# Kernel tuning notes

Hardware: AMD Instinct MI355X
Metric: run time of the kernel (lower is better)

Reference implementation:

```python
import jax, jax.numpy as jnp
import numpy as np

E = 128   # embedding_dim
H = 8     # num_attention_heads
D = 16    # head_size = E // H


def setup_inputs() -> dict:
    key = jax.random.key(0)
    ks = jax.random.split(key, 7)
    B, N = 2, 512
    x = jax.random.normal(ks[0], (B, N, E), jnp.float32)
    e = jax.random.uniform(ks[1], (B, N, N), jnp.float32)  # dense pairwise edge weights
    s_qkv = 1.0 / np.sqrt(D)
    w_qkv = jax.random.uniform(ks[2], (3 * H * D, E), jnp.float32, -s_qkv, s_qkv)
    w_ekv = jax.random.normal(ks[3], (2 * H * D, 1), jnp.float32) * 1.0
    b_ekv = jax.random.normal(ks[4], (2 * H * D,), jnp.float32) * 0.01
    s_prj = 1.0 / np.sqrt(E)
    w_prj = jax.random.uniform(ks[5], (E, H * D), jnp.float32, -s_prj, s_prj)
    b_prj = jnp.zeros((E,), jnp.float32)
    return {"x": x, "e": e, "w_qkv": w_qkv, "w_ekv": w_ekv,
            "b_ekv": b_ekv, "w_prj": w_prj, "b_prj": b_prj}


def reference(x, e, w_qkv, w_ekv, b_ekv, w_prj, b_prj):
    B, N, _ = x.shape
    # qkv projection: [B,N,3*H*D] split per einops '(S H D)'
    qkv = (x @ w_qkv.T).reshape(B, N, 3, H, D)
    q = jnp.transpose(qkv[:, :, 0], (0, 2, 1, 3))  # [B,H,N,D]
    k = jnp.transpose(qkv[:, :, 1], (0, 2, 1, 3))  # [B,H,N,D]
    v = jnp.transpose(qkv[:, :, 2], (0, 2, 1, 3))  # [B,H,N,D]
    # edge-conditioned K/V biases: Linear(1 -> 2HD) + LeakyReLU(0.01)
    ekv = jax.nn.leaky_relu(e[..., None] * w_ekv[:, 0] + b_ekv)  # [B,N,M,2HD]
    ekv = ekv.reshape(B, N, N, 2, H, D)
    ekm = jnp.transpose(ekv[..., 0, :, :], (0, 3, 1, 2, 4))  # [B,H,N,M,D]
    evm = jnp.transpose(ekv[..., 1, :, :], (0, 3, 1, 2, 4))  # [B,H,N,M,D]
    # dots[b,h,n,m] = q[b,h,n] . (k[b,h,n] + ekm[b,h,n,m])
    # NOTE: original uses the key of the *query* node n (broadcast over m).
    dots = jnp.sum(q * k, axis=-1)[..., None] \
        + jnp.einsum('bhnd,bhnmd->bhnm', q, ekm)
    attn = jax.nn.softmax(dots / np.sqrt(D), axis=-1)  # [B,H,N,M]
    # hat[b,h,n] = sum_m attn * (v[b,h,n] + evm[b,h,n,m])
    hat = v * jnp.sum(attn, axis=-1)[..., None] \
        + jnp.einsum('bhnm,bhnmd->bhnd', attn, evm)  # [B,H,N,D]
    out = jnp.transpose(hat, (0, 2, 1, 3)).reshape(B, N, H * D) @ w_prj.T + b_prj
    return out
```

## Files before the change

kernel.cpp:

```cpp
#include <hip/hip_runtime.h>
#include <math.h>

#define BATCH 2
#define NSEQ  512
#define EDIM  128
#define HNUM  8
#define DDIM  16
#define MROWS (BATCH*NSEQ)

__global__ __launch_bounds__(256)
void qkv_gemm(const float* __restrict__ x, const float* __restrict__ w,
              float* __restrict__ qkv) {
    __shared__ float4 As[32 * 32];
    __shared__ float4 Bs[64 * 32];

    const int tid  = threadIdx.x;
    const int row0 = blockIdx.y * 32;
    const int col0 = blockIdx.x * 64;

    #pragma unroll
    for (int it = 0; it < 4; ++it) {
        int idx = tid + it * 256;
        int r = idx >> 5, k4 = idx & 31;
        As[r * 32 + (k4 ^ ((r >> 2) & 7))] =
            ((const float4*)(x + (size_t)(row0 + r) * 128))[k4];
    }
    #pragma unroll
    for (int it = 0; it < 8; ++it) {
        int idx = tid + it * 256;
        int r = idx >> 5, k4 = idx & 31;
        Bs[r * 32 + (k4 ^ ((r >> 2) & 7))] =
            ((const float4*)(w + (size_t)(col0 + r) * 128))[k4];
    }
    __syncthreads();

    const int ty = tid >> 4;
    const int tx = tid & 15;
    const int ra  = ty * 2;
    const int swa = (ra >> 2) & 7;
    const int rb  = tx * 4;
    const int swb = tx & 7;

    float acc[2][4] = {};
    #pragma unroll
    for (int k4 = 0; k4 < 32; ++k4) {
        float4 a0 = As[ ra      * 32 + (k4 ^ swa)];
        float4 a1 = As[(ra + 1) * 32 + (k4 ^ swa)];
        float4 bv[4];
        #pragma unroll
        for (int j = 0; j < 4; ++j)
            bv[j] = Bs[(rb + j) * 32 + (k4 ^ swb)];
        #pragma unroll
        for (int j = 0; j < 4; ++j) {
            acc[0][j] = fmaf(a0.x, bv[j].x, acc[0][j]);
            acc[0][j] = fmaf(a0.y, bv[j].y, acc[0][j]);
            acc[0][j] = fmaf(a0.z, bv[j].z, acc[0][j]);
            acc[0][j] = fmaf(a0.w, bv[j].w, acc[0][j]);
            acc[1][j] = fmaf(a1.x, bv[j].x, acc[1][j]);
            acc[1][j] = fmaf(a1.y, bv[j].y, acc[1][j]);
            acc[1][j] = fmaf(a1.z, bv[j].z, acc[1][j]);
            acc[1][j] = fmaf(a1.w, bv[j].w, acc[1][j]);
        }
    }

    #pragma unroll
    for (int i = 0; i < 2; ++i) {
        float* crow = qkv + (size_t)(row0 + ra + i) * 384 + col0 + rb;
        *(float4*)crow = make_float4(acc[i][0], acc[i][1], acc[i][2], acc[i][3]);
    }
}

__global__ __launch_bounds__(512)
void attn_proj(const float* __restrict__ qkv, const float* __restrict__ e,
               const float* __restrict__ wekv, const float* __restrict__ bekv,
               const float* __restrict__ wprj, const float* __restrict__ bprj,
               float* __restrict__ out) {
    __shared__ float hat_s[EDIM];

    const int tid  = threadIdx.x;
    const int lane = tid & 63;
    const int h    = tid >> 6;
    const int bn   = blockIdx.x;

    const float* qrow = qkv + (size_t)bn * 384 + h * DDIM;
    const float* krow = qrow + EDIM;
    const float* vrow = qrow + 2 * EDIM;
    const float* erow = e + (size_t)bn * NSEQ;

    const float SC = 0.25f * 1.44269504088896340736f;

    float wk[DDIM], bk[DDIM], cd[DDIM];
    float qk = 0.f, qwk = 0.f, qbk = 0.f;
    #pragma unroll
    for (int d = 0; d < DDIM; ++d) {
        float q = qrow[d];
        qk  = fmaf(q, krow[d], qk);
        wk[d] = wekv[h * DDIM + d];
        bk[d] = bekv[h * DDIM + d];
        qwk = fmaf(q, wk[d], qwk);
        qbk = fmaf(q, bk[d], qbk);
        cd[d] = 0.495f * SC * q;
    }
    const float Alin = SC * 0.505f * qwk;
    const float base = SC * (qk + 0.505f * qbk);

    float dots[NSEQ / 64], ev[NSEQ / 64];
    float lmax = -1e30f;
    #pragma unroll
    for (int c = 0; c < NSEQ / 64; ++c) {
        float s = erow[c * 64 + lane];
        ev[c] = s;
        float dot = fmaf(s, Alin, base);
        #pragma unroll
        for (int d = 0; d < DDIM; ++d) {
            float t = fmaf(s, wk[d], bk[d]);
            dot = fmaf(cd[d], fabsf(t), dot);
        }
        dots[c] = dot;
        lmax = fmaxf(lmax, dot);
    }
    #pragma unroll
    for (int off = 32; off >= 1; off >>= 1)
        lmax = fmaxf(lmax, __shfl_xor(lmax, off, 64));

    float wvv[DDIM], bv[DDIM], racc[DDIM];
    #pragma unroll
    for (int d = 0; d < DDIM; ++d) {
        wvv[d]  = wekv[EDIM + h * DDIM + d];
        bv[d]   = bekv[EDIM + h * DDIM + d];
        racc[d] = 0.f;
    }
    float sp = 0.f, spe = 0.f;
    #pragma unroll
    for (int c = 0; c < NSEQ / 64; ++c) {
        float p = __builtin_amdgcn_exp2f(dots[c] - lmax);
        float s = ev[c];
        sp  += p;
        spe  = fmaf(p, s, spe);
        float pm = 0.495f * p;
        #pragma unroll
        for (int d = 0; d < DDIM; ++d) {
            float t = fmaf(s, wvv[d], bv[d]);
            racc[d] = fmaf(pm, fabsf(t), racc[d]);
        }
    }

    #pragma unroll
    for (int off = 1; off < 64; off <<= 1) {
        sp  += __shfl_xor(sp,  off, 64);
        spe += __shfl_xor(spe, off, 64);
        #pragma unroll
        for (int d = 0; d < DDIM; ++d)
            racc[d] += __shfl_xor(racc[d], off, 64);
    }

    float rsel = racc[0];
    #pragma unroll
    for (int d = 1; d < DDIM; ++d) rsel = (lane == d) ? racc[d] : rsel;
    if (lane < DDIM) {
        float wvs = wekv[EDIM + h * DDIM + lane];
        float bvs = bekv[EDIM + h * DDIM + lane];
        float acc = rsel + 0.505f * (fmaf(wvs, spe, bvs * sp));
        hat_s[h * DDIM + lane] = vrow[lane] + acc / sp;
    }
    __syncthreads();

    const int c    = tid >> 2;
    const int quad = tid & 3;
    const float4* wp = (const float4*)(wprj + (size_t)c * EDIM + quad * 32);
    const float4* hp = (const float4*)(hat_s + quad * 32);
    float s = 0.f;
    #pragma unroll
    for (int j = 0; j < 8; ++j) {
        float4 wv4 = wp[j], hv4 = hp[j];
        s = fmaf(wv4.x, hv4.x, s);
        s = fmaf(wv4.y, hv4.y, s);
        s = fmaf(wv4.z, hv4.z, s);
        s = fmaf(wv4.w, hv4.w, s);
    }
    s += __shfl_xor(s, 1, 64);
    s += __shfl_xor(s, 2, 64);
    if (quad == 0)
        out[(size_t)bn * EDIM + c] = s + bprj[c];
}

extern "C" void kernel_launch(void* const* d_in, const int* in_sizes, int n_in,
                              void* d_out, int out_size, void* d_ws, size_t ws_size,
                              hipStream_t stream) {
    const float* x     = (const float*)d_in[0];
    const float* e     = (const float*)d_in[1];
    const float* w_qkv = (const float*)d_in[2];
    const float* w_ekv = (const float*)d_in[3];
    const float* b_ekv = (const float*)d_in[4];
    const float* w_prj = (const float*)d_in[5];
    const float* b_prj = (const float*)d_in[6];
    float* out = (float*)d_out;

    float* qkv = (float*)d_ws;

    qkv_gemm<<<dim3(384 / 64, MROWS / 32), 256, 0, stream>>>(x, w_qkv, qkv);

    attn_proj<<<MROWS, 512, 0, stream>>>(qkv, e, w_ekv, b_ekv, w_prj, b_prj, out);
}
```

Before: 94.11 us.

## Fuse QKV projection into attention kernel, computing per-row GEMV in shared memory

```diff
diff --git a/kernel.cpp b/kernel.cpp
--- a/kernel.cpp
+++ b/kernel.cpp
@@ -8,73 +8,13 @@
 #define DDIM  16
 #define MROWS (BATCH*NSEQ)
 
-__global__ __launch_bounds__(256)
-void qkv_gemm(const float* __restrict__ x, const float* __restrict__ w,
-              float* __restrict__ qkv) {
-    __shared__ float4 As[32 * 32];
-    __shared__ float4 Bs[64 * 32];
-
-    const int tid  = threadIdx.x;
-    const int row0 = blockIdx.y * 32;
-    const int col0 = blockIdx.x * 64;
-
-    #pragma unroll
-    for (int it = 0; it < 4; ++it) {
-        int idx = tid + it * 256;
-        int r = idx >> 5, k4 = idx & 31;
-        As[r * 32 + (k4 ^ ((r >> 2) & 7))] =
-            ((const float4*)(x + (size_t)(row0 + r) * 128))[k4];
-    }
-    #pragma unroll
-    for (int it = 0; it < 8; ++it) {
-        int idx = tid + it * 256;
-        int r = idx >> 5, k4 = idx & 31;
-        Bs[r * 32 + (k4 ^ ((r >> 2) & 7))] =
-            ((const float4*)(w + (size_t)(col0 + r) * 128))[k4];
-    }
-    __syncthreads();
-
-    const int ty = tid >> 4;
-    const int tx = tid & 15;
-    const int ra  = ty * 2;
-    const int swa = (ra >> 2) & 7;
-    const int rb  = tx * 4;
-    const int swb = tx & 7;
-
-    float acc[2][4] = {};
-    #pragma unroll
-    for (int k4 = 0; k4 < 32; ++k4) {
-        float4 a0 = As[ ra      * 32 + (k4 ^ swa)];
-        float4 a1 = As[(ra + 1) * 32 + (k4 ^ swa)];
-        float4 bv[4];
-        #pragma unroll
-        for (int j = 0; j < 4; ++j)
-            bv[j] = Bs[(rb + j) * 32 + (k4 ^ swb)];
-        #pragma unroll
-        for (int j = 0; j < 4; ++j) {
-            acc[0][j] = fmaf(a0.x, bv[j].x, acc[0][j]);
-            acc[0][j] = fmaf(a0.y, bv[j].y, acc[0][j]);
-            acc[0][j] = fmaf(a0.z, bv[j].z, acc[0][j]);
-            acc[0][j] = fmaf(a0.w, bv[j].w, acc[0][j]);
-            acc[1][j] = fmaf(a1.x, bv[j].x, acc[1][j]);
-            acc[1][j] = fmaf(a1.y, bv[j].y, acc[1][j]);
-            acc[1][j] = fmaf(a1.z, bv[j].z, acc[1][j]);
-            acc[1][j] = fmaf(a1.w, bv[j].w, acc[1][j]);
-        }
-    }
-
-    #pragma unroll
-    for (int i = 0; i < 2; ++i) {
-        float* crow = qkv + (size_t)(row0 + ra + i) * 384 + col0 + rb;
-        *(float4*)crow = make_float4(acc[i][0], acc[i][1], acc[i][2], acc[i][3]);
-    }
-}
-
-__global__ __launch_bounds__(512)
-void attn_proj(const float* __restrict__ qkv, const float* __restrict__ e,
-               const float* __restrict__ wekv, const float* __restrict__ bekv,
-               const float* __restrict__ wprj, const float* __restrict__ bprj,
-               float* __restrict__ out) {
+__global__ __launch_bounds__(512, 4)
+void fused_attn(const float* __restrict__ x,    const float* __restrict__ e,
+                const float* __restrict__ wqkv, const float* __restrict__ wekv,
+                const float* __restrict__ bekv, const float* __restrict__ wprj,
+                const float* __restrict__ bprj, float* __restrict__ out) {
+    __shared__ float xs[EDIM];
+    __shared__ float qkvs[3 * EDIM];
     __shared__ float hat_s[EDIM];
 
     const int tid  = threadIdx.x;
@@ -82,10 +22,43 @@
     const int h    = tid >> 6;
     const int bn   = blockIdx.x;
 
-    const float* qrow = qkv + (size_t)bn * 384 + h * DDIM;
+    const float* erow = e + (size_t)bn * NSEQ;
+    float ev[NSEQ / 64];
+    #pragma unroll
+    for (int c = 0; c < NSEQ / 64; ++c)
+        ev[c] = erow[c * 64 + lane];
+
+    if (tid < 32)
+        ((float4*)xs)[tid] = ((const float4*)(x + (size_t)bn * EDIM))[tid];
+    __syncthreads();
+
+    {
+        const int o   = tid >> 2;
+        const int seg = tid & 3;
+        #pragma unroll
+        for (int rep = 0; rep < 3; ++rep) {
+            const int oo = o + rep * 128;
+            const float4* wp = (const float4*)(wqkv + (size_t)oo * EDIM + seg * 32);
+            const float4* xp = (const float4*)(xs + seg * 32);
+            float s = 0.f;
+            #pragma unroll
+            for (int j = 0; j < 8; ++j) {
+                float4 w4 = wp[j], x4 = xp[j];
+                s = fmaf(w4.x, x4.x, s);
+                s = fmaf(w4.y, x4.y, s);
+                s = fmaf(w4.z, x4.z, s);
+                s = fmaf(w4.w, x4.w, s);
+            }
+            s += __shfl_xor(s, 1, 64);
+            s += __shfl_xor(s, 2, 64);
+            if (seg == 0) qkvs[oo] = s;
+        }
+    }
+    __syncthreads();
+
+    const float* qrow = qkvs + h * DDIM;
     const float* krow = qrow + EDIM;
     const float* vrow = qrow + 2 * EDIM;
-    const float* erow = e + (size_t)bn * NSEQ;
 
     const float SC = 0.25f * 1.44269504088896340736f;
 
@@ -104,12 +77,11 @@
     const float Alin = SC * 0.505f * qwk;
     const float base = SC * (qk + 0.505f * qbk);
 
-    float dots[NSEQ / 64], ev[NSEQ / 64];
+    float dots[NSEQ / 64];
     float lmax = -1e30f;
     #pragma unroll
     for (int c = 0; c < NSEQ / 64; ++c) {
-        float s = erow[c * 64 + lane];
-        ev[c] = s;
+        float s = ev[c];
         float dot = fmaf(s, Alin, base);
         #pragma unroll
         for (int d = 0; d < DDIM; ++d) {
@@ -160,7 +132,7 @@
     if (lane < DDIM) {
         float wvs = wekv[EDIM + h * DDIM + lane];
         float bvs = bekv[EDIM + h * DDIM + lane];
-        float acc = rsel + 0.505f * (fmaf(wvs, spe, bvs * sp));
+        float acc = rsel + 0.505f * fmaf(wvs, spe, bvs * sp);
         hat_s[h * DDIM + lane] = vrow[lane] + acc / sp;
     }
     __syncthreads();
@@ -172,11 +144,11 @@
     float s = 0.f;
     #pragma unroll
     for (int j = 0; j < 8; ++j) {
-        float4 wv4 = wp[j], hv4 = hp[j];
-        s = fmaf(wv4.x, hv4.x, s);
-        s = fmaf(wv4.y, hv4.y, s);
-        s = fmaf(wv4.z, hv4.z, s);
-        s = fmaf(wv4.w, hv4.w, s);
+        float4 w4 = wp[j], h4 = hp[j];
+        s = fmaf(w4.x, h4.x, s);
+        s = fmaf(w4.y, h4.y, s);
+        s = fmaf(w4.z, h4.z, s);
+        s = fmaf(w4.w, h4.w, s);
     }
     s += __shfl_xor(s, 1, 64);
     s += __shfl_xor(s, 2, 64);
@@ -196,9 +168,6 @@
     const float* b_prj = (const float*)d_in[6];
     float* out = (float*)d_out;
 
-    float* qkv = (float*)d_ws;
-
-    qkv_gemm<<<dim3(384 / 64, MROWS / 32), 256, 0, stream>>>(x, w_qkv, qkv);
-
-    attn_proj<<<MROWS, 512, 0, stream>>>(qkv, e, w_ekv, b_ekv, w_prj, b_prj, out);
+    fused_attn<<<MROWS, 512, 0, stream>>>(x, e, w_qkv, w_ekv, b_ekv,
+                                          w_prj, b_prj, out);
 }
```

Measured after the change: 102.9 us. 9.4% more time.

## Drop K projection and softmax max pass; reduce racc via LDS transpose

Applied to the files above, without the earlier changes.

```diff
diff --git a/kernel.cpp b/kernel.cpp
--- a/kernel.cpp
+++ b/kernel.cpp
@@ -9,14 +9,16 @@
 #define MROWS (BATCH*NSEQ)
 
 __global__ __launch_bounds__(256)
-void qkv_gemm(const float* __restrict__ x, const float* __restrict__ w,
-              float* __restrict__ qkv) {
+void qv_gemm(const float* __restrict__ x, const float* __restrict__ w,
+             float* __restrict__ qv) {
     __shared__ float4 As[32 * 32];
     __shared__ float4 Bs[64 * 32];
 
     const int tid  = threadIdx.x;
     const int row0 = blockIdx.y * 32;
-    const int col0 = blockIdx.x * 64;
+    const int bx   = blockIdx.x;
+    const int wr0  = (bx >> 1) * 256 + (bx & 1) * 64;
+    const int cc0  = (bx >> 1) * 128 + (bx & 1) * 64;
 
     #pragma unroll
     for (int it = 0; it < 4; ++it) {
@@ -30,12 +32,12 @@
         int idx = tid + it * 256;
         int r = idx >> 5, k4 = idx & 31;
         Bs[r * 32 + (k4 ^ ((r >> 2) & 7))] =
-            ((const float4*)(w + (size_t)(col0 + r) * 128))[k4];
+            ((const float4*)(w + (size_t)(wr0 + r) * 128))[k4];
     }
     __syncthreads();
 
-    const int ty = tid >> 4;
-    const int tx = tid & 15;
+    const int ty  = tid >> 4;
+    const int tx  = tid & 15;
     const int ra  = ty * 2;
     const int swa = (ra >> 2) & 7;
     const int rb  = tx * 4;
@@ -46,102 +48,87 @@
     for (int k4 = 0; k4 < 32; ++k4) {
         float4 a0 = As[ ra      * 32 + (k4 ^ swa)];
         float4 a1 = As[(ra + 1) * 32 + (k4 ^ swa)];
-        float4 bv[4];
+        float4 bv4[4];
         #pragma unroll
         for (int j = 0; j < 4; ++j)
-            bv[j] = Bs[(rb + j) * 32 + (k4 ^ swb)];
+            bv4[j] = Bs[(rb + j) * 32 + (k4 ^ swb)];
         #pragma unroll
         for (int j = 0; j < 4; ++j) {
-            acc[0][j] = fmaf(a0.x, bv[j].x, acc[0][j]);
-            acc[0][j] = fmaf(a0.y, bv[j].y, acc[0][j]);
-            acc[0][j] = fmaf(a0.z, bv[j].z, acc[0][j]);
-            acc[0][j] = fmaf(a0.w, bv[j].w, acc[0][j]);
-            acc[1][j] = fmaf(a1.x, bv[j].x, acc[1][j]);
-            acc[1][j] = fmaf(a1.y, bv[j].y, acc[1][j]);
-            acc[1][j] = fmaf(a1.z, bv[j].z, acc[1][j]);
-            acc[1][j] = fmaf(a1.w, bv[j].w, acc[1][j]);
+            acc[0][j] = fmaf(a0.x, bv4[j].x, acc[0][j]);
+            acc[0][j] = fmaf(a0.y, bv4[j].y, acc[0][j]);
+            acc[0][j] = fmaf(a0.z, bv4[j].z, acc[0][j]);
+            acc[0][j] = fmaf(a0.w, bv4[j].w, acc[0][j]);
+            acc[1][j] = fmaf(a1.x, bv4[j].x, acc[1][j]);
+            acc[1][j] = fmaf(a1.y, bv4[j].y, acc[1][j]);
+            acc[1][j] = fmaf(a1.z, bv4[j].z, acc[1][j]);
+            acc[1][j] = fmaf(a1.w, bv4[j].w, acc[1][j]);
         }
     }
 
     #pragma unroll
     for (int i = 0; i < 2; ++i) {
-        float* crow = qkv + (size_t)(row0 + ra + i) * 384 + col0 + rb;
+        float* crow = qv + (size_t)(row0 + ra + i) * 256 + cc0 + rb;
         *(float4*)crow = make_float4(acc[i][0], acc[i][1], acc[i][2], acc[i][3]);
     }
 }
 
 __global__ __launch_bounds__(512)
-void attn_proj(const float* __restrict__ qkv, const float* __restrict__ e,
+void attn_proj(const float* __restrict__ qv,   const float* __restrict__ e,
                const float* __restrict__ wekv, const float* __restrict__ bekv,
                const float* __restrict__ wprj, const float* __restrict__ bprj,
                float* __restrict__ out) {
     __shared__ float hat_s[EDIM];
+    __shared__ float red[HNUM][DDIM][65];
 
     const int tid  = threadIdx.x;
     const int lane = tid & 63;
-    const int h    = tid >> 6;
+    const int h    = __builtin_amdgcn_readfirstlane(tid >> 6);
     const int bn   = blockIdx.x;
 
-    const float* qrow = qkv + (size_t)bn * 384 + h * DDIM;
-    const float* krow = qrow + EDIM;
-    const float* vrow = qrow + 2 * EDIM;
+    const float* qrow = qv + (size_t)bn * 256 + h * DDIM;
+    const float* vrow = qrow + 128;
     const float* erow = e + (size_t)bn * NSEQ;
 
     const float SC = 0.25f * 1.44269504088896340736f;
 
-    float wk[DDIM], bk[DDIM], cd[DDIM];
-    float qk = 0.f, qwk = 0.f, qbk = 0.f;
+    float wk[DDIM], bk[DDIM], cd[DDIM], wvv[DDIM], bv[DDIM];
+    float qwk = 0.f;
     #pragma unroll
     for (int d = 0; d < DDIM; ++d) {
         float q = qrow[d];
-        qk  = fmaf(q, krow[d], qk);
-        wk[d] = wekv[h * DDIM + d];
-        bk[d] = bekv[h * DDIM + d];
-        qwk = fmaf(q, wk[d], qwk);
-        qbk = fmaf(q, bk[d], qbk);
-        cd[d] = 0.495f * SC * q;
+        wk[d]  = wekv[h * DDIM + d];
+        bk[d]  = bekv[h * DDIM + d];
+        wvv[d] = wekv[EDIM + h * DDIM + d];
+        bv[d]  = bekv[EDIM + h * DDIM + d];
+        qwk    = fmaf(q, wk[d], qwk);
+        cd[d]  = 0.495f * SC * q;
     }
     const float Alin = SC * 0.505f * qwk;
-    const float base = SC * (qk + 0.505f * qbk);
 
-    float dots[NSEQ / 64], ev[NSEQ / 64];
-    float lmax = -1e30f;
+    float4 e0 = ((const float4*)erow)[lane];
+    float4 e1 = ((const float4*)erow)[lane + 64];
+    float evs[8] = {e0.x, e0.y, e0.z, e0.w, e1.x, e1.y, e1.z, e1.w};
+
+    float racc[DDIM];
     #pragma unroll
-    for (int c = 0; c < NSEQ / 64; ++c) {
-        float s = erow[c * 64 + lane];
-        ev[c] = s;
-        float dot = fmaf(s, Alin, base);
+    for (int d = 0; d < DDIM; ++d) racc[d] = 0.f;
+    float sp = 0.f, spe = 0.f;
+    #pragma unroll
+    for (int c = 0; c < 8; ++c) {
+        float s = evs[c];
+        float dot = s * Alin;
         #pragma unroll
         for (int d = 0; d < DDIM; ++d) {
             float t = fmaf(s, wk[d], bk[d]);
             dot = fmaf(cd[d], fabsf(t), dot);
         }
-        dots[c] = dot;
-        lmax = fmaxf(lmax, dot);
-    }
-    #pragma unroll
-    for (int off = 32; off >= 1; off >>= 1)
-        lmax = fmaxf(lmax, __shfl_xor(lmax, off, 64));
-
-    float wvv[DDIM], bv[DDIM], racc[DDIM];
-    #pragma unroll
-    for (int d = 0; d < DDIM; ++d) {
-        wvv[d]  = wekv[EDIM + h * DDIM + d];
-        bv[d]   = bekv[EDIM + h * DDIM + d];
-        racc[d] = 0.f;
-    }
-    float sp = 0.f, spe = 0.f;
-    #pragma unroll
-    for (int c = 0; c < NSEQ / 64; ++c) {
-        float p = __builtin_amdgcn_exp2f(dots[c] - lmax);
-        float s = ev[c];
+        float p = __builtin_amdgcn_exp2f(dot);
         sp  += p;
         spe  = fmaf(p, s, spe);
-        float pm = 0.495f * p;
         #pragma unroll
         for (int d = 0; d < DDIM; ++d) {
             float t = fmaf(s, wvv[d], bv[d]);
-            racc[d] = fmaf(pm, fabsf(t), racc[d]);
+            racc[d] = fmaf(p, fabsf(t), racc[d]);
         }
     }
 
@@ -149,18 +136,24 @@
     for (int off = 1; off < 64; off <<= 1) {
         sp  += __shfl_xor(sp,  off, 64);
         spe += __shfl_xor(spe, off, 64);
-        #pragma unroll
-        for (int d = 0; d < DDIM; ++d)
-            racc[d] += __shfl_xor(racc[d], off, 64);
     }
 
-    float rsel = racc[0];
     #pragma unroll
-    for (int d = 1; d < DDIM; ++d) rsel = (lane == d) ? racc[d] : rsel;
+    for (int d = 0; d < DDIM; ++d)
+        red[h][d][lane] = racc[d];
+    __syncthreads();
+    const int rc = lane & 15, rg = lane >> 4;
+    float part = 0.f;
+    #pragma unroll
+    for (int j = 0; j < 16; ++j)
+        part += red[h][rc][rg * 16 + j];
+    part += __shfl_xor(part, 16, 64);
+    part += __shfl_xor(part, 32, 64);
+
     if (lane < DDIM) {
         float wvs = wekv[EDIM + h * DDIM + lane];
         float bvs = bekv[EDIM + h * DDIM + lane];
-        float acc = rsel + 0.505f * (fmaf(wvs, spe, bvs * sp));
+        float acc = 0.495f * part + 0.505f * fmaf(wvs, spe, bvs * sp);
         hat_s[h * DDIM + lane] = vrow[lane] + acc / sp;
     }
     __syncthreads();
@@ -172,11 +165,11 @@
     float s = 0.f;
     #pragma unroll
     for (int j = 0; j < 8; ++j) {
-        float4 wv4 = wp[j], hv4 = hp[j];
-        s = fmaf(wv4.x, hv4.x, s);
-        s = fmaf(wv4.y, hv4.y, s);
-        s = fmaf(wv4.z, hv4.z, s);
-        s = fmaf(wv4.w, hv4.w, s);
+        float4 w4 = wp[j], h4 = hp[j];
+        s = fmaf(w4.x, h4.x, s);
+        s = fmaf(w4.y, h4.y, s);
+        s = fmaf(w4.z, h4.z, s);
+        s = fmaf(w4.w, h4.w, s);
     }
     s += __shfl_xor(s, 1, 64);
     s += __shfl_xor(s, 2, 64);
@@ -196,9 +189,9 @@
     const float* b_prj = (const float*)d_in[6];
     float* out = (float*)d_out;
 
-    float* qkv = (float*)d_ws;
+    float* qv = (float*)d_ws;
 
-    qkv_gemm<<<dim3(384 / 64, MROWS / 32), 256, 0, stream>>>(x, w_qkv, qkv);
+    qv_gemm<<<dim3(4, MROWS / 32), 256, 0, stream>>>(x, w_qkv, qv);
 
-    attn_proj<<<MROWS, 512, 0, stream>>>(qkv, e, w_ekv, b_ekv, w_prj, b_prj, out);
+    attn_proj<<<MROWS, 512, 0, stream>>>(qv, e, w_ekv, b_ekv, w_prj, b_prj, out);
 }
```

After: 90.84 us. 1.04x faster.
